# Kernel tuning notes

Hardware: AMD Instinct MI355X
Metric: run time of the kernel (lower is better)

Reference implementation:

```python
import jax, jax.numpy as jnp
import numpy as np

B, C1, C2, H, W, NH = 16, 256, 256, 64, 64, 8
C = C2 // 2          # hidden dim of retention blocks (c2*e)
HD = C // NH         # head dim
EPS = 1e-5           # torch BatchNorm2d / LayerNorm default eps


def _ln(x, g, b):
    mu = jnp.mean(x, -1, keepdims=True)
    var = jnp.mean((x - mu) ** 2, -1, keepdims=True)
    return (x - mu) * jax.lax.rsqrt(var + EPS) * g + b


def _bn_silu(y, g, b, m, v):
    # inference-mode BatchNorm2d (running stats) + SiLU, channels axis=1
    y = (y - m[:, None, None]) * jax.lax.rsqrt(v + EPS)[:, None, None] * g[:, None, None] + b[:, None, None]
    return jax.nn.silu(y)


def _decay1d(L, dec):
    # RelPos2d.generate_1d_decay: exp(decay_n * |i-j|), shape (NH, L, L)
    idx = jnp.arange(L)
    m = jnp.abs(idx[:, None] - idx[None, :]).astype(jnp.float32)
    return jnp.exp(dec[:, None, None] * m)


def setup_inputs() -> dict:
    key = jax.random.key(0)
    ks = jax.random.split(key, 8)
    s = 0.02
    return {
        'x': jax.random.normal(ks[0], (B, C1, H, W), jnp.float32),
        'cv1_w': jax.random.normal(ks[1], (2 * C, C1), jnp.float32) * s,
        'bn1_g': jnp.ones((2 * C,)), 'bn1_b': jnp.zeros((2 * C,)),
        'bn1_m': jnp.zeros((2 * C,)), 'bn1_v': jnp.ones((2 * C,)),
        'cv2_w': jax.random.normal(ks[2], (C2, 3 * C), jnp.float32) * s,
        'bn2_g': jnp.ones((C2,)), 'bn2_b': jnp.zeros((C2,)),
        'bn2_m': jnp.zeros((C2,)), 'bn2_v': jnp.ones((C2,)),
        'ln1_g': jnp.ones((C,)), 'ln1_b': jnp.zeros((C,)),
        'qkv_w': jax.random.normal(ks[3], (3 * C, C), jnp.float32) * s,
        'qkv_b': jnp.zeros((3 * C,)),
        'proj_w': jax.random.normal(ks[4], (C, C), jnp.float32) * s,
        'proj_b': jnp.zeros((C,)),
        'gamma': jnp.ones((C,)),
        'ln2_g': jnp.ones((C,)), 'ln2_b': jnp.zeros((C,)),
        'ffn_w1': jax.random.normal(ks[5], (2 * C, C), jnp.float32) * s,
        'ffn_b1': jnp.zeros((2 * C,)),
        'ffn_w2': jax.random.normal(ks[6], (C, 2 * C), jnp.float32) * s,
        'ffn_b2': jnp.zeros((C,)),
    }


def reference(x, cv1_w, bn1_g, bn1_b, bn1_m, bn1_v, cv2_w, bn2_g, bn2_b, bn2_m, bn2_v,
              ln1_g, ln1_b, qkv_w, qkv_b, proj_w, proj_b, gamma,
              ln2_g, ln2_b, ffn_w1, ffn_b1, ffn_w2, ffn_b2):
    # RelPos2d: decay per head, initial_value=2, heads_range=4; mode='chunk' -> 1D decays
    dec = jnp.log(1.0 - 2.0 ** (-2.0 - 4.0 * jnp.arange(NH, dtype=jnp.float32) / NH))
    decay_h = _decay1d(H, dec)  # (NH, H, H)
    decay_w = _decay1d(W, dec)  # (NH, W, W)

    # cv1: 1x1 conv + BN + SiLU, then chunk into two halves of C channels
    y = _bn_silu(jnp.einsum('bchw,oc->bohw', x, cv1_w), bn1_g, bn1_b, bn1_m, bn1_v)
    y1, y2 = y[:, :C], y[:, C:]

    # RetBlock on channels-last feature map
    f = jnp.transpose(y2, (0, 2, 3, 1))  # (B,H,W,C)
    res = f
    fn = _ln(f, ln1_g, ln1_b)
    qkv = fn @ qkv_w.T + qkv_b
    q, k, v = jnp.split(qkv, 3, axis=-1)

    def heads(t):
        return jnp.transpose(t.reshape(B, H, W, NH, HD), (0, 3, 1, 2, 4))  # (B,NH,H,W,HD)

    q, k, v = heads(q), heads(k), heads(v)

    # axial retention: row attention with exponential row-decay
    qk_h = jnp.einsum('bnhwc,bnHwc->bnhHw', q, k) * decay_h[None, :, :, :, None]
    out_h = jnp.einsum('bnhHw,bnHwc->bnhwc', qk_h, v)
    # column attention with exponential column-decay
    qk_w = jnp.einsum('bnhwc,bnhWc->bnhwW', q, k) * decay_w[None, :, None, :, :]
    out_w = jnp.einsum('bnhwW,bnhWc->bnhwc', qk_w, v)
    out = 0.5 * (out_h + out_w)
    out = jnp.transpose(out, (0, 2, 3, 1, 4)).reshape(B, H, W, C)

    f = res + (out @ proj_w.T + proj_b) * gamma
    res2 = f
    fn2 = _ln(f, ln2_g, ln2_b)
    h1 = jax.nn.gelu(fn2 @ ffn_w1.T + ffn_b1, approximate=False)
    f = res2 + (h1 @ ffn_w2.T + ffn_b2)

    f = jnp.transpose(f, (0, 3, 1, 2))  # back to (B,C,H,W)
    cat = jnp.concatenate([y1, y2, f], axis=1)  # (B,3C,H,W)
    return _bn_silu(jnp.einsum('bchw,oc->bohw', cat, cv2_w), bn2_g, bn2_b, bn2_m, bn2_v)
```

## Files before the change

kernel.cpp:

```cpp
#include <hip/hip_runtime.h>
#include <math.h>

#define LEPS 1e-5f
static constexpr int NPOS = 65536;

typedef __attribute__((ext_vector_type(8))) short short8;
typedef __attribute__((ext_vector_type(4))) float floatx4;

__device__ __forceinline__ ushort f2bf(float f) {
    unsigned int u = __float_as_uint(f);
    u += 0x7FFF + ((u >> 16) & 1);
    return (ushort)(u >> 16);
}
__device__ __forceinline__ float bfu(ushort h) {
    return __uint_as_float((unsigned int)h << 16);
}
__device__ __forceinline__ float bfl(unsigned int u) {
    return __uint_as_float(u << 16);
}
__device__ __forceinline__ float bfh(unsigned int u) {
    return __uint_as_float(u & 0xffff0000u);
}

typedef __attribute__((address_space(1))) const unsigned int gu32_t;
typedef __attribute__((address_space(3))) unsigned int lu32_t;
__device__ __forceinline__ void gld16(const ushort* g, ushort* l) {
    __builtin_amdgcn_global_load_lds((gu32_t*)g, (lu32_t*)l, 16, 0, 0);
}

struct WcvtArgs { const float* src[6]; ushort* dst[6]; int n[6]; };
__global__ __launch_bounds__(256)
void wcvt_k(WcvtArgs a)
{
    const int seg = blockIdx.y;
    const float* s = a.src[seg];
    ushort* d = a.dst[seg];
    const int n = a.n[seg];
    for (int i = blockIdx.x * 256 + threadIdx.x; i < n; i += gridDim.x * 256)
        d[i] = f2bf(s[i]);
}

__global__ __launch_bounds__(256)
void bnprep_k(const float* g1, const float* b1, const float* m1, const float* v1,
              const float* g2, const float* b2, const float* m2, const float* v2,
              float* s1, float* h1, float* s2, float* h2)
{
    const int i = threadIdx.x;
    if (blockIdx.x == 0) {
        const float s = g1[i] * rsqrtf(v1[i] + LEPS);
        s1[i] = s; h1[i] = b1[i] - m1[i] * s;
    } else {
        const float s = g2[i] * rsqrtf(v2[i] + LEPS);
        s2[i] = s; h2[i] = b2[i] - m2[i] * s;
    }
}

__global__ __launch_bounds__(256)
void tr_k(const float* __restrict__ x, ushort* __restrict__ xT)
{
    __shared__ float tile[64][65];
    const int t = threadIdx.x;
    const int bi = blockIdx.x;
    const int hwt = bi & 63, ct = (bi >> 6) & 3, b = bi >> 8;
    const int p0 = b * 4096 + hwt * 64, c0 = ct * 64;
    const float* src = x + ((size_t)(b * 256 + c0) << 12) + hwt * 64;
#pragma unroll
    for (int i = 0; i < 16; i++) {
        int cc = (t >> 6) + i * 4;
        tile[cc][t & 63] = src[((size_t)cc << 12) + (t & 63)];
    }
    __syncthreads();
    const int c2 = (t & 31) * 2;
    const int pr = t >> 5;
#pragma unroll
    for (int i = 0; i < 8; i++) {
        int pp = pr + i * 8;
        unsigned int u = (unsigned int)f2bf(tile[c2][pp])
                       | ((unsigned int)f2bf(tile[c2 + 1][pp]) << 16);
        *(unsigned int*)&xT[(size_t)(p0 + pp) * 256 + c0 + c2] = u;
    }
}

template<int KDIM, int ARS, int AMODE, int EPI, int LN>
__global__ __launch_bounds__(256)
void gemm_k(const ushort* __restrict__ A0, const ushort* __restrict__ A1,
            const ushort* __restrict__ Wm, const float* __restrict__ bias,
            const float* __restrict__ q0, const float* __restrict__ q1,
            const ushort* __restrict__ resh,
            const float* __restrict__ lng, const float* __restrict__ lnb,
            ushort* __restrict__ lnout, void* __restrict__ outv, int ors)
{
    __shared__ __align__(16) ushort smem[128 * 136];
    ushort* As = smem;
    ushort* Bs = smem + 128 * 64;
    const int t = threadIdx.x;
    const int p0 = blockIdx.x * 128;
    const int o0 = blockIdx.y * 128;
    const int lane = t & 63, wv = t >> 6;
    const int wm = (wv & 1) * 64, wn = (wv >> 1) * 64;
    const int ln15 = lane & 15, quad = lane >> 4;
    const int dl_row = lane >> 3;
    const int dl_sch = (lane & 7) ^ dl_row;
    const int c_off0 = ((quad) ^ (ln15 & 7)) * 8;
    const int c_off1 = ((4 + quad) ^ (ln15 & 7)) * 8;
    floatx4 acc[4][4] = {};

    for (int k0 = 0; k0 < KDIM; k0 += 64) {
        if (AMODE == 3) {
            const int row = t >> 1, half = t & 1;
            const ushort* s1 = A0 + (size_t)(p0 + row) * 128 + k0 + half * 32;
            const ushort* s2 = A1 + (size_t)(p0 + row) * 128 + k0 + half * 32;
#pragma unroll
            for (int i = 0; i < 4; i++) {
                uint4 ua = ((const uint4*)s1)[i];
                uint4 ub = ((const uint4*)s2)[i];
                const unsigned int* ap = (const unsigned int*)&ua;
                const unsigned int* bp = (const unsigned int*)&ub;
                uint4 w;
                unsigned int* wp = (unsigned int*)&w;
#pragma unroll
                for (int j = 0; j < 4; j++)
                    wp[j] = (unsigned int)f2bf(0.5f * (bfl(ap[j]) + bfl(bp[j])))
                          | ((unsigned int)f2bf(0.5f * (bfh(ap[j]) + bfh(bp[j]))) << 16);
                const int pch = (half * 4 + i) ^ (row & 7);
                *(uint4*)&As[row * 64 + pch * 8] = w;
            }
        } else {
#pragma unroll
            for (int i = 0; i < 4; i++) {
                const int r0 = wv * 32 + i * 8;
                const int row = r0 + dl_row;
                const ushort* src;
                if (AMODE == 2) {
                    if (k0 < 256) src = A0 + (size_t)(p0 + row) * 256 + k0 + dl_sch * 8;
                    else          src = A1 + (size_t)(p0 + row) * 128 + (k0 - 256) + dl_sch * 8;
                } else {
                    src = A0 + (size_t)(p0 + row) * ARS + k0 + dl_sch * 8;
                }
                gld16(src, &As[r0 * 64]);
            }
        }
#pragma unroll
        for (int i = 0; i < 4; i++) {
            const int r0 = wv * 32 + i * 8;
            gld16(Wm + (size_t)(o0 + r0 + dl_row) * KDIM + k0 + dl_sch * 8, &Bs[r0 * 64]);
        }
        __syncthreads();
#pragma unroll
        for (int kh = 0; kh < 2; kh++) {
            const int co = kh ? c_off1 : c_off0;
            short8 a[4], b[4];
#pragma unroll
            for (int i = 0; i < 4; i++)
                a[i] = *(const short8*)&As[(wm + i * 16 + ln15) * 64 + co];
#pragma unroll
            for (int j = 0; j < 4; j++)
                b[j] = *(const short8*)&Bs[(wn + j * 16 + ln15) * 64 + co];
#pragma unroll
            for (int i = 0; i < 4; i++)
#pragma unroll
                for (int j = 0; j < 4; j++)
                    acc[i][j] = __builtin_amdgcn_mfma_f32_16x16x32_bf16(
                        a[i], b[j], acc[i][j], 0, 0, 0);
        }
        __syncthreads();
    }

    if (EPI == 2) {
        float* cb = (float*)smem;
        float* ob = (float*)outv + (((size_t)(p0 >> 12) * 256) << 12);
        const int hw0 = p0 & 4095;
#pragma unroll
        for (int chunk = 0; chunk < 2; chunk++) {
            __syncthreads();
            if ((wn >> 6) == chunk) {
#pragma unroll
                for (int i = 0; i < 4; i++)
#pragma unroll
                for (int j = 0; j < 4; j++) {
                    const int ch = j * 16 + ln15;
                    const int o = o0 + chunk * 64 + ch;
                    const float sc = q0[o], sh = q1[o];
#pragma unroll
                    for (int r = 0; r < 4; r++) {
                        const int pos = wm + i * 16 + quad * 4 + r;
                        float v = acc[i][j][r] * sc + sh;
                        v = v / (1.f + __expf(-v));
                        cb[ch * 132 + pos] = v;
                    }
                }
            }
            __syncthreads();
#pragma unroll
            for (int it = 0; it < 8; it++) {
                const int flat = it * 1024 + t * 4;
                const int ch = flat >> 7, pos = flat & 127;
                const int o = o0 + chunk * 64 + ch;
                float4 v4 = *(const float4*)&cb[ch * 132 + pos];
                *(float4*)&ob[((size_t)o << 12) + hw0 + pos] = v4;
            }
        }
        return;
    }

    const bool lnact = LN && (EPI != 1 || o0 == 128);
    ushort (*lt)[136] = (ushort (*)[136])smem;
#pragma unroll
    for (int i = 0; i < 4; i++) {
#pragma unroll
        for (int r = 0; r < 4; r++) {
            const int lr = wm + i * 16 + quad * 4 + r;
            const int p = p0 + lr;
#pragma unroll
            for (int j = 0; j < 4; j++) {
                const int ol = wn + j * 16 + ln15;
                const int o = o0 + ol;
                float v = acc[i][j][r];
                if (EPI == 0) {
                    v += bias[o];
                } else if (EPI == 1) {
                    v = v * q0[o] + q1[o];
                    v = v / (1.f + __expf(-v));
                } else if (EPI == 4) {
                    v = bfu(resh[(size_t)p * 256 + 128 + o]) + (v + bias[o]) * q0[o];
                }
                lt[lr][ol] = f2bf(v);
            }
        }
    }
    __syncthreads();
    {
        ushort* o16 = (ushort*)outv;
#pragma unroll
        for (int it = 0; it < 8; it++) {
            const int flat = it * 256 + t;
            const int row = flat >> 4, ch = (flat & 15) * 8;
            *(uint4*)&o16[(size_t)(p0 + row) * (size_t)ors + o0 + ch] =
                *(const uint4*)&lt[row][ch];
        }
    }

    if (lnact) {
        const int rrow = t >> 1, rhalf = t & 1;
        const ushort* rp = &lt[rrow][rhalf * 64];
        float s = 0.f, s2 = 0.f;
#pragma unroll
        for (int i = 0; i < 8; i++) {
            const uint4 u = *(const uint4*)(rp + i * 8);
            const unsigned int ww[4] = {u.x, u.y, u.z, u.w};
#pragma unroll
            for (int j = 0; j < 4; j++) {
                const float a = bfl(ww[j]), c = bfh(ww[j]);
                s += a + c; s2 += a * a + c * c;
            }
        }
        s += __shfl_xor(s, 1); s2 += __shfl_xor(s2, 1);
        const float mu = s * (1.f / 128.f);
        const float rn = rsqrtf(s2 * (1.f / 128.f) - mu * mu + LEPS);
        ushort* op = lnout + (size_t)(p0 + rrow) * 128 + rhalf * 64;
#pragma unroll
        for (int i = 0; i < 8; i++) {
            const uint4 u = *(const uint4*)(rp + i * 8);
            const unsigned int ww[4] = {u.x, u.y, u.z, u.w};
            uint4 wout;
            unsigned int* wo = (unsigned int*)&wout;
#pragma unroll
            for (int j = 0; j < 4; j++) {
                const int ch = rhalf * 64 + i * 8 + j * 2;
                const float2 gg = *(const float2*)(lng + ch);
                const float2 bb = *(const float2*)(lnb + ch);
                const float a = (bfl(ww[j]) - mu) * rn * gg.x + bb.x;
                const float c = (bfh(ww[j]) - mu) * rn * gg.y + bb.y;
                wo[j] = (unsigned int)f2bf(a) | ((unsigned int)f2bf(c) << 16);
            }
            *(uint4*)(op + i * 8) = wout;
        }
    }
}

__global__ __launch_bounds__(256)
void ffn_k(const ushort* __restrict__ fn2, const ushort* __restrict__ w1,
           const float* __restrict__ b1, const ushort* __restrict__ w2,
           const float* __restrict__ b2, ushort* __restrict__ f)
{
    __shared__ __align__(16) ushort smem[64 * 64 + 256 * 64 + 64 * 264];
    ushort* Ax = smem;
    ushort* Wt = smem + 64 * 64;
    ushort (*H1)[264] = (ushort (*)[264])(smem + 64 * 64 + 256 * 64);
    const int t = threadIdx.x;
    const int p0 = blockIdx.x * 64;
    const int lane = t & 63, wv = t >> 6;
    const int ln15 = lane & 15, quad = lane >> 4;
    const int dl_row = lane >> 3;
    const int dl_sch = (lane & 7) ^ dl_row;
    const int c_off0 = ((quad) ^ (ln15 & 7)) * 8;
    const int c_off1 = ((4 + quad) ^ (ln15 & 7)) * 8;

    floatx4 acc1[4][4] = {};
    for (int k0 = 0; k0 < 128; k0 += 64) {
#pragma unroll
        for (int i = 0; i < 2; i++) {
            const int r0 = wv * 16 + i * 8;
            gld16(fn2 + (size_t)(p0 + r0 + dl_row) * 128 + k0 + dl_sch * 8, &Ax[r0 * 64]);
        }
#pragma unroll
        for (int i = 0; i < 8; i++) {
            const int r0 = wv * 64 + i * 8;
            gld16(w1 + (size_t)(r0 + dl_row) * 128 + k0 + dl_sch * 8, &Wt[r0 * 64]);
        }
        __syncthreads();
#pragma unroll
        for (int kh = 0; kh < 2; kh++) {
            const int co = kh ? c_off1 : c_off0;
            short8 a[4], b[4];
#pragma unroll
            for (int i = 0; i < 4; i++)
                a[i] = *(const short8*)&Ax[(i * 16 + ln15) * 64 + co];
#pragma unroll
            for (int j = 0; j < 4; j++)
                b[j] = *(const short8*)&Wt[(wv * 64 + j * 16 + ln15) * 64 + co];
#pragma unroll
            for (int i = 0; i < 4; i++)
#pragma unroll
                for (int j = 0; j < 4; j++)
                    acc1[i][j] = __builtin_amdgcn_mfma_f32_16x16x32_bf16(
                        a[i], b[j], acc1[i][j], 0, 0, 0);
        }
        __syncthreads();
    }
    {
        float bb1[4];
#pragma unroll
        for (int j = 0; j < 4; j++) bb1[j] = b1[wv * 64 + j * 16 + ln15];
#pragma unroll
        for (int i = 0; i < 4; i++)
#pragma unroll
        for (int j = 0; j < 4; j++)
#pragma unroll
        for (int r = 0; r < 4; r++) {
            float v = acc1[i][j][r] + bb1[j];
            v = 0.5f * v * (1.f + erff(v * 0.70710678118654752f));
            H1[i * 16 + quad * 4 + r][wv * 64 + j * 16 + ln15] = f2bf(v);
        }
    }
    __syncthreads();

    floatx4 acc2[4][2] = {};
    for (int k0 = 0; k0 < 256; k0 += 64) {
#pragma unroll
        for (int i = 0; i < 4; i++) {
            const int r0 = wv * 32 + i * 8;
            gld16(w2 + (size_t)(r0 + dl_row) * 256 + k0 + dl_sch * 8, &Wt[r0 * 64]);
        }
        __syncthreads();
#pragma unroll
        for (int kh = 0; kh < 2; kh++) {
            const int co = kh ? c_off1 : c_off0;
            short8 a[4], b[2];
#pragma unroll
            for (int i = 0; i < 4; i++)
                a[i] = *(const short8*)&H1[i * 16 + ln15][k0 + kh * 32 + quad * 8];
#pragma unroll
            for (int j = 0; j < 2; j++)
                b[j] = *(const short8*)&Wt[(wv * 32 + j * 16 + ln15) * 64 + co];
#pragma unroll
            for (int i = 0; i < 4; i++)
#pragma unroll
                for (int j = 0; j < 2; j++)
                    acc2[i][j] = __builtin_amdgcn_mfma_f32_16x16x32_bf16(
                        a[i], b[j], acc2[i][j], 0, 0, 0);
        }
        __syncthreads();
    }

    ushort* Ft = smem;
#pragma unroll
    for (int i = 0; i < 4; i++) {
        const int r0 = wv * 16 + i * 4;
        gld16(f + (size_t)(p0 + r0 + (lane >> 4)) * 128 + (lane & 15) * 8, &Ft[r0 * 128]);
    }
    __syncthreads();
    {
        float bb2[2];
#pragma unroll
        for (int j = 0; j < 2; j++) bb2[j] = b2[wv * 32 + j * 16 + ln15];
#pragma unroll
        for (int i = 0; i < 4; i++)
#pragma unroll
        for (int r = 0; r < 4; r++) {
            const int pos = i * 16 + quad * 4 + r;
#pragma unroll
            for (int j = 0; j < 2; j++) {
                const int ch = wv * 32 + j * 16 + ln15;
                const int idx = pos * 128 + ch;
                Ft[idx] = f2bf(bfu(Ft[idx]) + acc2[i][j][r] + bb2[j]);
            }
        }
    }
    __syncthreads();
#pragma unroll
    for (int it = 0; it < 4; it++) {
        const int flat = it * 256 + t;
        const int row = flat >> 4, ch = (flat & 15) * 8;
        *(uint4*)&f[(size_t)(p0 + row) * 128 + ch] = *(const uint4*)&Ft[row * 128 + ch];
    }
}

__global__ __launch_bounds__(256)
void attn_k(const ushort* __restrict__ qkv, ushort* __restrict__ oh,
            ushort* __restrict__ ow)
{
    __shared__ ushort VtS[4][16 * 72];
    __shared__ ushort SbS[4][64 * 72];
    __shared__ float dpow[128];
    const int t = threadIdx.x, wv = t >> 6, lane = t & 63;
    const int ln15 = lane & 15, quad = lane >> 4;
    const int dirH = (blockIdx.y == 0);
    ushort* outb = dirH ? oh : ow;
    const int blk = blockIdx.x;
    const int lg = blk & 15, n = (blk >> 4) & 7, b = blk >> 7;
    if (t < 128) {
        const float dec = logf(1.f - exp2f(-2.f - 0.5f * (float)n));
        int d = t - 63; if (d < 0) d = -d;
        dpow[t] = __expf(dec * (float)d);
    }
    const int fixed = lg * 4 + wv;
    const int stride = dirH ? 64 : 1;
    const size_t base = (size_t)b * 4096 + (dirH ? fixed : fixed * 64);
    const size_t cbase = base * 384 + n * 16;

    {
        const ushort* vp = qkv + cbase + (size_t)lane * stride * 384 + 256;
        const uint4 va = *(const uint4*)vp, vb = *(const uint4*)(vp + 8);
        ushort* vt = VtS[wv] + lane;
        const unsigned int w[8] = { va.x, va.y, va.z, va.w, vb.x, vb.y, vb.z, vb.w };
#pragma unroll
        for (int d = 0; d < 8; d++) {
            vt[(2 * d) * 72]     = (ushort)(w[d] & 0xffff);
            vt[(2 * d + 1) * 72] = (ushort)(w[d] >> 16);
        }
    }
    short8 qa[4], kb[4];
    {
        const short8 z = {0, 0, 0, 0, 0, 0, 0, 0};
#pragma unroll
        for (int mt = 0; mt < 4; mt++) {
            const int i = mt * 16 + ln15;
            if (quad < 2) {
                const ushort* qp = qkv + cbase + (size_t)i * stride * 384 + quad * 8;
                qa[mt] = *(const short8*)qp;
                kb[mt] = *(const short8*)(qp + 128);
            } else { qa[mt] = z; kb[mt] = z; }
        }
    }
    __syncthreads();

#pragma unroll
    for (int mt = 0; mt < 4; mt++) {
#pragma unroll
        for (int nt = 0; nt < 4; nt++) {
            floatx4 c = {0.f, 0.f, 0.f, 0.f};
            c = __builtin_amdgcn_mfma_f32_16x16x32_bf16(qa[mt], kb[nt], c, 0, 0, 0);
            const int i0 = mt * 16 + quad * 4;
            const int jl = nt * 16 + ln15;
            const float* lut = dpow + (i0 - jl + 63);
            ushort* sb = SbS[wv] + i0 * 72 + jl;
#pragma unroll
            for (int r = 0; r < 4; r++)
                sb[r * 72] = f2bf(c[r] * lut[r]);
        }
    }
    __syncthreads();

    short8 av[2];
#pragma unroll
    for (int c = 0; c < 2; c++)
        av[c] = *(const short8*)&VtS[wv][ln15 * 72 + c * 32 + quad * 8];
    floatx4 o[4] = {};
#pragma unroll
    for (int nt4 = 0; nt4 < 4; nt4++) {
#pragma unroll
        for (int c = 0; c < 2; c++) {
            const short8 bs = *(const short8*)
                &SbS[wv][(nt4 * 16 + ln15) * 72 + c * 32 + quad * 8];
            o[nt4] = __builtin_amdgcn_mfma_f32_16x16x32_bf16(av[c], bs, o[nt4], 0, 0, 0);
        }
    }
#pragma unroll
    for (int nt4 = 0; nt4 < 4; nt4++) {
        const int i = nt4 * 16 + ln15;
        ushort* op = outb + (base + (size_t)i * stride) * 128 + n * 16 + quad * 4;
        uint2 w;
        w.x = (unsigned int)f2bf(o[nt4][0]) | ((unsigned int)f2bf(o[nt4][1]) << 16);
        w.y = (unsigned int)f2bf(o[nt4][2]) | ((unsigned int)f2bf(o[nt4][3]) << 16);
        *(uint2*)op = w;
    }
}

extern "C" void kernel_launch(void* const* d_in, const int* in_sizes, int n_in,
                              void* d_out, int out_size, void* d_ws, size_t ws_size,
                              hipStream_t stream)
{
    const float* x      = (const float*)d_in[0];
    const float* cv1_w  = (const float*)d_in[1];
    const float* bn1_g  = (const float*)d_in[2];
    const float* bn1_b  = (const float*)d_in[3];
    const float* bn1_m  = (const float*)d_in[4];
    const float* bn1_v  = (const float*)d_in[5];
    const float* cv2_w  = (const float*)d_in[6];
    const float* bn2_g  = (const float*)d_in[7];
    const float* bn2_b  = (const float*)d_in[8];
    const float* bn2_m  = (const float*)d_in[9];
    const float* bn2_v  = (const float*)d_in[10];
    const float* ln1_g  = (const float*)d_in[11];
    const float* ln1_b  = (const float*)d_in[12];
    const float* qkv_w  = (const float*)d_in[13];
    const float* qkv_b  = (const float*)d_in[14];
    const float* proj_w = (const float*)d_in[15];
    const float* proj_b = (const float*)d_in[16];
    const float* gamma  = (const float*)d_in[17];
    const float* ln2_g  = (const float*)d_in[18];
    const float* ln2_b  = (const float*)d_in[19];
    const float* ffn_w1 = (const float*)d_in[20];
    const float* ffn_b1 = (const float*)d_in[21];
    const float* ffn_w2 = (const float*)d_in[22];
    const float* ffn_b2 = (const float*)d_in[23];

    ushort* W = (ushort*)d_ws;
    ushort* y    = W;
    ushort* f    = y    + (size_t)NPOS * 256;
    ushort* tmp  = f    + (size_t)NPOS * 128;
    ushort* owb  = tmp  + (size_t)NPOS * 128;
    ushort* qkvb = owb  + (size_t)NPOS * 128;
    ushort* xT   = qkvb + (size_t)NPOS * 384;
    ushort* wc1  = xT   + (size_t)NPOS * 256;
    ushort* wqkv = wc1  + 65536;
    ushort* wpr  = wqkv + 49152;
    ushort* ww1  = wpr  + 16384;
    ushort* ww2  = ww1  + 32768;
    ushort* wc2  = ww2  + 32768;
    float*  bns1 = (float*)(wc2 + 98304);
    float*  bnb1 = bns1 + 256;
    float*  bns2 = bnb1 + 256;
    float*  bnb2 = bns2 + 256;
    float*  out  = (float*)d_out;

    WcvtArgs wa;
    wa.src[0] = cv1_w;  wa.dst[0] = wc1;  wa.n[0] = 65536;
    wa.src[1] = qkv_w;  wa.dst[1] = wqkv; wa.n[1] = 49152;
    wa.src[2] = proj_w; wa.dst[2] = wpr;  wa.n[2] = 16384;
    wa.src[3] = ffn_w1; wa.dst[3] = ww1;  wa.n[3] = 32768;
    wa.src[4] = ffn_w2; wa.dst[4] = ww2;  wa.n[4] = 32768;
    wa.src[5] = cv2_w;  wa.dst[5] = wc2;  wa.n[5] = 98304;
    wcvt_k<<<dim3(96, 6), 256, 0, stream>>>(wa);
    bnprep_k<<<2, 256, 0, stream>>>(bn1_g, bn1_b, bn1_m, bn1_v,
                                    bn2_g, bn2_b, bn2_m, bn2_v,
                                    bns1, bnb1, bns2, bnb2);
    tr_k<<<4096, 256, 0, stream>>>(x, xT);

    gemm_k<256, 256, 0, 1, 1><<<dim3(512, 2), 256, 0, stream>>>(
        xT, nullptr, wc1, nullptr, bns1, bnb1, nullptr, ln1_g, ln1_b, tmp, y, 256);
    gemm_k<128, 128, 0, 0, 0><<<dim3(512, 3), 256, 0, stream>>>(
        tmp, nullptr, wqkv, qkv_b, nullptr, nullptr, nullptr, nullptr, nullptr,
        nullptr, qkvb, 384);
    attn_k<<<dim3(2048, 2), 256, 0, stream>>>(qkvb, tmp, owb);
    gemm_k<128, 128, 3, 4, 1><<<dim3(512, 1), 256, 0, stream>>>(
        tmp, owb, wpr, proj_b, gamma, nullptr, y, ln2_g, ln2_b, tmp, f, 128);
    ffn_k<<<1024, 256, 0, stream>>>(tmp, ww1, ffn_b1, ww2, ffn_b2, f);
    gemm_k<384, 0, 2, 2, 0><<<dim3(512, 2), 256, 0, stream>>>(
        y, f, wc2, nullptr, bns2, bnb2, nullptr, nullptr, nullptr, nullptr, out, 0);
}
```

Before: 355.7 us.

## Double-buffer GEMM and FFN shared-memory tiles to overlap loads with MFMA

The generic GEMM kernel now keeps two shared-memory buffers for the A and W tiles and issues the next K-tile's global-to-LDS loads before computing the current one. It uses explicit waitcnt and barriers instead of __syncthreads. In the AMODE 3 path, the averaged A operand is prefetched into registers for the next tile. The FFN kernel likewise double-buffers the second-layer weight tiles, prefetches the first one during the GELU epilogue, overlaps the residual load with the last MFMA step, and hoists the bias loads. The extra buffering increases shared-memory use (64KB for the GEMM), which may lower occupancy, and the hand-written vmcnt counts must match the number of outstanding loads exactly.

```diff
diff --git a/kernel.cpp b/kernel.cpp
--- a/kernel.cpp
+++ b/kernel.cpp
@@ -90,9 +90,8 @@
             const float* __restrict__ lng, const float* __restrict__ lnb,
             ushort* __restrict__ lnout, void* __restrict__ outv, int ors)
 {
-    __shared__ __align__(16) ushort smem[128 * 136];
-    ushort* As = smem;
-    ushort* Bs = smem + 128 * 64;
+    constexpr int NT = KDIM / 64;
+    __shared__ __align__(16) ushort smem[4 * 128 * 64];
     const int t = threadIdx.x;
     const int p0 = blockIdx.x * 128;
     const int o0 = blockIdx.y * 128;
@@ -105,57 +104,63 @@
     const int c_off1 = ((4 + quad) ^ (ln15 & 7)) * 8;
     floatx4 acc[4][4] = {};
 
-    for (int k0 = 0; k0 < KDIM; k0 += 64) {
-        if (AMODE == 3) {
-            const int row = t >> 1, half = t & 1;
-            const ushort* s1 = A0 + (size_t)(p0 + row) * 128 + k0 + half * 32;
-            const ushort* s2 = A1 + (size_t)(p0 + row) * 128 + k0 + half * 32;
-#pragma unroll
-            for (int i = 0; i < 4; i++) {
-                uint4 ua = ((const uint4*)s1)[i];
-                uint4 ub = ((const uint4*)s2)[i];
-                const unsigned int* ap = (const unsigned int*)&ua;
-                const unsigned int* bp = (const unsigned int*)&ub;
-                uint4 w;
-                unsigned int* wp = (unsigned int*)&w;
-#pragma unroll
-                for (int j = 0; j < 4; j++)
-                    wp[j] = (unsigned int)f2bf(0.5f * (bfl(ap[j]) + bfl(bp[j])))
-                          | ((unsigned int)f2bf(0.5f * (bfh(ap[j]) + bfh(bp[j]))) << 16);
-                const int pch = (half * 4 + i) ^ (row & 7);
-                *(uint4*)&As[row * 64 + pch * 8] = w;
-            }
-        } else {
-#pragma unroll
-            for (int i = 0; i < 4; i++) {
-                const int r0 = wv * 32 + i * 8;
-                const int row = r0 + dl_row;
-                const ushort* src;
-                if (AMODE == 2) {
-                    if (k0 < 256) src = A0 + (size_t)(p0 + row) * 256 + k0 + dl_sch * 8;
-                    else          src = A1 + (size_t)(p0 + row) * 128 + (k0 - 256) + dl_sch * 8;
-                } else {
-                    src = A0 + (size_t)(p0 + row) * ARS + k0 + dl_sch * 8;
-                }
-                gld16(src, &As[r0 * 64]);
-            }
-        }
+    const int a3row = t >> 1, a3half = t & 1;
+    uint4 ra[4], rb4[4];
+
+    auto stageA = [&](int k0, int bc) {
 #pragma unroll
         for (int i = 0; i < 4; i++) {
             const int r0 = wv * 32 + i * 8;
-            gld16(Wm + (size_t)(o0 + r0 + dl_row) * KDIM + k0 + dl_sch * 8, &Bs[r0 * 64]);
-        }
-        __syncthreads();
+            const int row = r0 + dl_row;
+            const ushort* src;
+            if (AMODE == 2) {
+                if (k0 < 256) src = A0 + (size_t)(p0 + row) * 256 + k0 + dl_sch * 8;
+                else          src = A1 + (size_t)(p0 + row) * 128 + (k0 - 256) + dl_sch * 8;
+            } else {
+                src = A0 + (size_t)(p0 + row) * ARS + k0 + dl_sch * 8;
+            }
+            gld16(src, &smem[bc * 8192 + r0 * 64]);
+        }
+    };
+    auto stageB = [&](int k0, int bc) {
+#pragma unroll
+        for (int i = 0; i < 4; i++) {
+            const int r0 = wv * 32 + i * 8;
+            gld16(Wm + (size_t)(o0 + r0 + dl_row) * KDIM + k0 + dl_sch * 8,
+                  &smem[16384 + bc * 8192 + r0 * 64]);
+        }
+    };
+    auto loadA3 = [&](int k0) {
+        const ushort* s1 = A0 + (size_t)(p0 + a3row) * 128 + k0 + a3half * 32;
+        const ushort* s2 = A1 + (size_t)(p0 + a3row) * 128 + k0 + a3half * 32;
+#pragma unroll
+        for (int i = 0; i < 4; i++) { ra[i] = ((const uint4*)s1)[i]; rb4[i] = ((const uint4*)s2)[i]; }
+    };
+    auto writeA3 = [&](int bc) {
+#pragma unroll
+        for (int i = 0; i < 4; i++) {
+            const unsigned int* ap = (const unsigned int*)&ra[i];
+            const unsigned int* bp = (const unsigned int*)&rb4[i];
+            uint4 w; unsigned int* wp = (unsigned int*)&w;
+#pragma unroll
+            for (int j = 0; j < 4; j++)
+                wp[j] = (unsigned int)f2bf(0.5f * (bfl(ap[j]) + bfl(bp[j])))
+                      | ((unsigned int)f2bf(0.5f * (bfh(ap[j]) + bfh(bp[j]))) << 16);
+            const int pch = (a3half * 4 + i) ^ (a3row & 7);
+            *(uint4*)&smem[bc * 8192 + a3row * 64 + pch * 8] = w;
+        }
+    };
+    auto compute = [&](int bc) {
 #pragma unroll
         for (int kh = 0; kh < 2; kh++) {
             const int co = kh ? c_off1 : c_off0;
             short8 a[4], b[4];
 #pragma unroll
             for (int i = 0; i < 4; i++)
-                a[i] = *(const short8*)&As[(wm + i * 16 + ln15) * 64 + co];
+                a[i] = *(const short8*)&smem[bc * 8192 + (wm + i * 16 + ln15) * 64 + co];
 #pragma unroll
             for (int j = 0; j < 4; j++)
-                b[j] = *(const short8*)&Bs[(wn + j * 16 + ln15) * 64 + co];
+                b[j] = *(const short8*)&smem[16384 + bc * 8192 + (wn + j * 16 + ln15) * 64 + co];
 #pragma unroll
             for (int i = 0; i < 4; i++)
 #pragma unroll
@@ -163,7 +168,46 @@
                     acc[i][j] = __builtin_amdgcn_mfma_f32_16x16x32_bf16(
                         a[i], b[j], acc[i][j], 0, 0, 0);
         }
-        __syncthreads();
+    };
+
+    if (AMODE == 3) {
+        loadA3(0);
+        stageB(0, 0);
+#pragma unroll
+        for (int tt = 0; tt < NT; ++tt) {
+            const int cur = tt & 1;
+            writeA3(cur);
+            if (tt + 1 < NT) {
+                loadA3((tt + 1) * 64);
+                stageB((tt + 1) * 64, cur ^ 1);
+                asm volatile("s_waitcnt vmcnt(12) lgkmcnt(0)" ::: "memory");
+            } else {
+                asm volatile("s_waitcnt vmcnt(0) lgkmcnt(0)" ::: "memory");
+            }
+            __builtin_amdgcn_s_barrier();
+            __builtin_amdgcn_sched_barrier(0);
+            compute(cur);
+            __builtin_amdgcn_sched_barrier(0);
+            __builtin_amdgcn_s_barrier();
+        }
+    } else {
+        stageA(0, 0); stageB(0, 0);
+#pragma unroll
+        for (int tt = 0; tt < NT; ++tt) {
+            const int cur = tt & 1;
+            if (tt + 1 < NT) {
+                stageA((tt + 1) * 64, cur ^ 1);
+                stageB((tt + 1) * 64, cur ^ 1);
+                asm volatile("s_waitcnt vmcnt(8)" ::: "memory");
+            } else {
+                asm volatile("s_waitcnt vmcnt(0)" ::: "memory");
+            }
+            __builtin_amdgcn_s_barrier();
+            __builtin_amdgcn_sched_barrier(0);
+            compute(cur);
+            __builtin_amdgcn_sched_barrier(0);
+            __builtin_amdgcn_s_barrier();
+        }
     }
 
     if (EPI == 2) {
@@ -296,6 +340,12 @@
     const int c_off0 = ((quad) ^ (ln15 & 7)) * 8;
     const int c_off1 = ((4 + quad) ^ (ln15 & 7)) * 8;
 
+    float bb1[4], bb2[2];
+#pragma unroll
+    for (int j = 0; j < 4; j++) bb1[j] = b1[wv * 64 + j * 16 + ln15];
+#pragma unroll
+    for (int j = 0; j < 2; j++) bb2[j] = b2[wv * 32 + j * 16 + ln15];
+
     floatx4 acc1[4][4] = {};
     for (int k0 = 0; k0 < 128; k0 += 64) {
 #pragma unroll
@@ -328,10 +378,12 @@
         }
         __syncthreads();
     }
+#pragma unroll
+    for (int i = 0; i < 4; i++) {
+        const int r0 = wv * 32 + i * 8;
+        gld16(w2 + (size_t)(r0 + dl_row) * 256 + dl_sch * 8, &Wt[r0 * 64]);
+    }
     {
-        float bb1[4];
-#pragma unroll
-        for (int j = 0; j < 4; j++) bb1[j] = b1[wv * 64 + j * 16 + ln15];
 #pragma unroll
         for (int i = 0; i < 4; i++)
 #pragma unroll
@@ -343,26 +395,43 @@
             H1[i * 16 + quad * 4 + r][wv * 64 + j * 16 + ln15] = f2bf(v);
         }
     }
-    __syncthreads();
+    asm volatile("s_waitcnt lgkmcnt(0)" ::: "memory");
+    __builtin_amdgcn_s_barrier();
+    __builtin_amdgcn_sched_barrier(0);
 
     floatx4 acc2[4][2] = {};
-    for (int k0 = 0; k0 < 256; k0 += 64) {
-#pragma unroll
-        for (int i = 0; i < 4; i++) {
-            const int r0 = wv * 32 + i * 8;
-            gld16(w2 + (size_t)(r0 + dl_row) * 256 + k0 + dl_sch * 8, &Wt[r0 * 64]);
-        }
-        __syncthreads();
+#pragma unroll
+    for (int t4 = 0; t4 < 4; ++t4) {
+        const int cur = t4 & 1;
+        if (t4 + 1 < 4) {
+#pragma unroll
+            for (int i = 0; i < 4; i++) {
+                const int r0 = wv * 32 + i * 8;
+                gld16(w2 + (size_t)(r0 + dl_row) * 256 + (t4 + 1) * 64 + dl_sch * 8,
+                      &Wt[(cur ^ 1) * 8192 + r0 * 64]);
+            }
+            asm volatile("s_waitcnt vmcnt(4)" ::: "memory");
+        } else {
+#pragma unroll
+            for (int i = 0; i < 4; i++) {
+                const int r0 = wv * 16 + i * 4;
+                gld16(f + (size_t)(p0 + r0 + (lane >> 4)) * 128 + (lane & 15) * 8,
+                      &smem[r0 * 128]);
+            }
+            asm volatile("s_waitcnt vmcnt(4)" ::: "memory");
+        }
+        __builtin_amdgcn_s_barrier();
+        __builtin_amdgcn_sched_barrier(0);
 #pragma unroll
         for (int kh = 0; kh < 2; kh++) {
             const int co = kh ? c_off1 : c_off0;
             short8 a[4], b[2];
 #pragma unroll
             for (int i = 0; i < 4; i++)
-                a[i] = *(const short8*)&H1[i * 16 + ln15][k0 + kh * 32 + quad * 8];
+                a[i] = *(const short8*)&H1[i * 16 + ln15][t4 * 64 + kh * 32 + quad * 8];
 #pragma unroll
             for (int j = 0; j < 2; j++)
-                b[j] = *(const short8*)&Wt[(wv * 32 + j * 16 + ln15) * 64 + co];
+                b[j] = *(const short8*)&Wt[cur * 8192 + (wv * 32 + j * 16 + ln15) * 64 + co];
 #pragma unroll
             for (int i = 0; i < 4; i++)
 #pragma unroll
@@ -370,20 +439,14 @@
                     acc2[i][j] = __builtin_amdgcn_mfma_f32_16x16x32_bf16(
                         a[i], b[j], acc2[i][j], 0, 0, 0);
         }
-        __syncthreads();
-    }
+        __builtin_amdgcn_sched_barrier(0);
+        __builtin_amdgcn_s_barrier();
+    }
+    asm volatile("s_waitcnt vmcnt(0)" ::: "memory");
+    __builtin_amdgcn_s_barrier();
 
     ushort* Ft = smem;
-#pragma unroll
-    for (int i = 0; i < 4; i++) {
-        const int r0 = wv * 16 + i * 4;
-        gld16(f + (size_t)(p0 + r0 + (lane >> 4)) * 128 + (lane & 15) * 8, &Ft[r0 * 128]);
-    }
-    __syncthreads();
     {
-        float bb2[2];
-#pragma unroll
-        for (int j = 0; j < 2; j++) bb2[j] = b2[wv * 32 + j * 16 + ln15];
 #pragma unroll
         for (int i = 0; i < 4; i++)
 #pragma unroll
```

Result: faster. 338.5 us (-4.8%).
